# Kernel optimization log

Hardware: AMD Instinct MI355X
Metric: run time of the kernel (lower is better)

## Reference

```python
import jax, jax.numpy as jnp
import numpy as np

B, C, H, W = 4, 192, 56, 56
D_STATE, D_CONV, EXPAND = 16, 3, 2
D_INNER = EXPAND * C
DT_RANK = (C + 15) // 16  # 12


def setup_inputs() -> dict:
    key = jax.random.key(0)
    ks = jax.random.split(key, 16)
    s = 0.02
    return {
        "x": jax.random.normal(ks[0], (B, C, H, W), jnp.float32),
        "ln1_g": jnp.ones((C,), jnp.float32),
        "ln1_b": jnp.zeros((C,), jnp.float32),
        "in_proj_w": jax.random.normal(ks[1], (2 * D_INNER, C), jnp.float32) * s,
        "conv1d_w": jax.random.normal(ks[2], (D_INNER, 1, D_CONV), jnp.float32) * s,
        "conv1d_b": jnp.zeros((D_INNER,), jnp.float32),
        "x_proj_w": jax.random.normal(ks[3], (DT_RANK + 2 * D_STATE, D_INNER), jnp.float32) * s,
        "dt_proj_w": jax.random.normal(ks[4], (D_INNER, DT_RANK), jnp.float32) * (DT_RANK ** -0.5),
        "dt_proj_b": jax.random.uniform(ks[5], (D_INNER,), jnp.float32, -4.6, -2.3),
        "A_log": jnp.tile(jnp.log(jnp.arange(1, D_STATE + 1, dtype=jnp.float32)), (D_INNER, 1)),
        "Dskip": jnp.ones((D_INNER,), jnp.float32),
        "out_proj_w": jax.random.normal(ks[6], (C, D_INNER), jnp.float32) * s,
        "dw_w": jax.random.normal(ks[7], (C, 1, 3, 3), jnp.float32) * s,
        "bn_g": jnp.ones((C,), jnp.float32),
        "bn_b": jnp.zeros((C,), jnp.float32),
        "bn_mean": jax.random.normal(ks[8], (C,), jnp.float32) * 0.1,
        "bn_var": jax.random.uniform(ks[9], (C,), jnp.float32, 0.5, 1.5),
        "ln2_g": jnp.ones((C,), jnp.float32),
        "ln2_b": jnp.zeros((C,), jnp.float32),
        "mlp_w1": jax.random.normal(ks[10], (4 * C, C), jnp.float32) * s,
        "mlp_b1": jnp.zeros((4 * C,), jnp.float32),
        "mlp_w2": jax.random.normal(ks[11], (C, 4 * C), jnp.float32) * s,
        "mlp_b2": jnp.zeros((C,), jnp.float32),
    }


def _ln(x, g, b, eps=1e-5):
    m = jnp.mean(x, -1, keepdims=True)
    v = jnp.var(x, -1, keepdims=True)
    return (x - m) * jax.lax.rsqrt(v + eps) * g + b


def _gelu(x):
    return jax.nn.gelu(x, approximate=False)


def _mamba(xf, in_proj_w, conv1d_w, conv1d_b, x_proj_w, dt_proj_w, dt_proj_b, A_log, Dskip, out_proj_w):
    # xf: (B, L, C) tokens
    Bn, L, _ = xf.shape
    xz = jnp.einsum('blc,ec->ble', xf, in_proj_w)  # (B, L, 2*d_inner)
    xm, z = jnp.split(xz, 2, axis=-1)
    # causal depthwise conv1d over L
    xm_t = jnp.transpose(xm, (0, 2, 1))  # (B, d_inner, L)
    conv = jax.lax.conv_general_dilated(
        xm_t, conv1d_w, (1,), [(D_CONV - 1, 0)],
        feature_group_count=D_INNER,
        dimension_numbers=('NCH', 'OIH', 'NCH'))
    xm = jax.nn.silu(jnp.transpose(conv + conv1d_b[None, :, None], (0, 2, 1)))  # (B, L, d_inner)
    x_dbl = jnp.einsum('bld,ed->ble', xm, x_proj_w)
    dt = x_dbl[..., :DT_RANK]
    Bm = x_dbl[..., DT_RANK:DT_RANK + D_STATE]   # (B, L, n)
    Cm = x_dbl[..., DT_RANK + D_STATE:]          # (B, L, n)
    delta = jax.nn.softplus(jnp.einsum('blr,dr->bld', dt, dt_proj_w) + dt_proj_b)
    A = -jnp.exp(A_log)                           # (d_inner, n)
    deltaA = jnp.exp(delta[..., None] * A)        # (B, L, d, n)
    deltaBx = (delta * xm)[..., None] * Bm[:, :, None, :]  # (B, L, d, n)

    def step(h, inp):
        dA, dBx, Ct = inp
        h = dA * h + dBx                          # (B, d, n)
        y = jnp.einsum('bdn,bn->bd', h, Ct)
        return h, y

    h0 = jnp.zeros((Bn, D_INNER, D_STATE), xm.dtype)
    _, ys = jax.lax.scan(step, h0, (jnp.transpose(deltaA, (1, 0, 2, 3)),
                                    jnp.transpose(deltaBx, (1, 0, 2, 3)),
                                    jnp.transpose(Cm, (1, 0, 2))))
    y = jnp.transpose(ys, (1, 0, 2)) + xm * Dskip  # (B, L, d_inner)
    y = y * jax.nn.silu(z)
    return jnp.einsum('bld,cd->blc', y, out_proj_w)


def reference(x, ln1_g, ln1_b, in_proj_w, conv1d_w, conv1d_b, x_proj_w, dt_proj_w, dt_proj_b,
              A_log, Dskip, out_proj_w, dw_w, bn_g, bn_b, bn_mean, bn_var,
              ln2_g, ln2_b, mlp_w1, mlp_b1, mlp_w2, mlp_b2):
    Bn, Cn, Hn, Wn = x.shape
    # --- branch 1: LN -> SS2D (Mamba over flattened tokens) + skip
    t = jnp.transpose(x, (0, 2, 3, 1))            # (B, H, W, C)
    t = _ln(t, ln1_g, ln1_b)
    tokens = t.reshape(Bn, Hn * Wn, Cn)           # row-major = rearrange 'b c h w -> b (h w) c' after LN
    y = _mamba(tokens, in_proj_w, conv1d_w, conv1d_b, x_proj_w, dt_proj_w, dt_proj_b,
               A_log, Dskip, out_proj_w)
    x1 = x + jnp.transpose(y.reshape(Bn, Hn, Wn, Cn), (0, 3, 1, 2))
    # --- branch 2: depthwise conv -> BN(eval) -> GELU + skip
    dw = jax.lax.conv_general_dilated(x1, dw_w, (1, 1), [(1, 1), (1, 1)],
                                      feature_group_count=Cn,
                                      dimension_numbers=('NCHW', 'OIHW', 'NCHW'))
    bn = (dw - bn_mean[None, :, None, None]) * jax.lax.rsqrt(bn_var + 1e-5)[None, :, None, None]
    bn = bn * bn_g[None, :, None, None] + bn_b[None, :, None, None]
    x2 = x1 + _gelu(bn)
    # --- branch 3: LN -> MLP + skip
    t = jnp.transpose(x2, (0, 2, 3, 1))
    t = _ln(t, ln2_g, ln2_b)
    h = _gelu(jnp.einsum('bhwc,ec->bhwe', t, mlp_w1) + mlp_b1)
    m = jnp.einsum('bhwe,ce->bhwc', h, mlp_w2) + mlp_b2
    return x2 + jnp.transpose(m, (0, 3, 1, 2))
```

## Files before the change

### kernel.cpp

```cpp
#include <hip/hip_runtime.h>
#include <hip/hip_bf16.h>
#include <math.h>

#define BATCH 4
#define CCH   192
#define HH    56
#define WW    56
#define LSEQ  (HH*WW)
#define NTOK  (BATCH*LSEQ)
#define DST   16
#define DIN   384
#define DTR   12
#define NXC   416
#define CL    32
#define NC    (LSEQ/CL)

typedef __attribute__((ext_vector_type(8))) short short8;
typedef __attribute__((ext_vector_type(4))) short short4v;
typedef __attribute__((ext_vector_type(4))) float floatx4;

__device__ __forceinline__ float siluf(float x)  { return x / (1.f + __expf(-x)); }
__device__ __forceinline__ float geluf(float x)  { return 0.5f * x * (1.f + erff(x * 0.70710678118654752f)); }
__device__ __forceinline__ float softplusf(float x) { return (x > 20.f) ? x : log1pf(__expf(x)); }
__device__ __forceinline__ float bf2f(short u) {
    union { unsigned int i; float f; } cv; cv.i = ((unsigned int)(unsigned short)u) << 16; return cv.f;
}
__device__ __forceinline__ short f2bf_bits(float v) {
    __hip_bfloat16 h = __float2bfloat16(v);
    return *(short*)&h;
}

#define WSZ0 147456
#define WSZ2 73728
#define WSZ3 147456
#define WSZ4 147456
__global__ __launch_bounds__(256) void cvt_weights(const float* __restrict__ w0,
                                                   const float* __restrict__ w2, const float* __restrict__ w3,
                                                   const float* __restrict__ w4,
                                                   __hip_bfloat16* __restrict__ o0,
                                                   __hip_bfloat16* __restrict__ o2, __hip_bfloat16* __restrict__ o3,
                                                   __hip_bfloat16* __restrict__ o4) {
    int i = blockIdx.x * 256 + threadIdx.x;
    if (i < WSZ0) { o0[i] = __float2bfloat16(w0[i]); return; } i -= WSZ0;
    if (i < WSZ2) { o2[i] = __float2bfloat16(w2[i]); return; } i -= WSZ2;
    if (i < WSZ3) { o3[i] = __float2bfloat16(w3[i]); return; } i -= WSZ3;
    if (i < WSZ4) { o4[i] = __float2bfloat16(w4[i]); }
}

__global__ __launch_bounds__(256) void make_wcomb(const float* __restrict__ xp_w,
                                                  const float* __restrict__ dt_w,
                                                  __hip_bfloat16* __restrict__ wcomb) {
    int i = blockIdx.x * 256 + threadIdx.x;
    if (i >= NXC * DIN) return;
    int row = i / DIN, k = i % DIN;
    float v;
    if (row < DIN) {
        v = 0.f;
#pragma unroll
        for (int r = 0; r < DTR; r++) v += dt_w[row * DTR + r] * xp_w[r * DIN + k];
    } else {
        v = xp_w[(row - DIN + DTR) * DIN + k];
    }
    wcomb[i] = __float2bfloat16(v);
}

__global__ __launch_bounds__(256) void ln_kernel(const float* __restrict__ x,
                                                 const float* __restrict__ g,
                                                 const float* __restrict__ bta,
                                                 __hip_bfloat16* __restrict__ out) {
    __shared__ float tile[CCH * 65];
    __shared__ float gs[CCH], bs[CCH];
    int t = threadIdx.x;
    int b = blockIdx.y, hw0 = blockIdx.x * 64;
    const float* xb = x + (size_t)b * CCH * LSEQ + hw0;
#pragma unroll 8
    for (int k = 0; k < 48; k++) {
        int idx = k * 256 + t;
        int c = idx >> 6, w = idx & 63;
        tile[c * 65 + w] = xb[(size_t)c * LSEQ + w];
    }
    if (t < CCH) { gs[t] = g[t]; bs[t] = bta[t]; }
    __syncthreads();
    int lane = t & 63, wave = t >> 6;
    int tk = lane & 15, p = lane >> 4;
    int tok = wave * 16 + tk;
    float s = 0.f, s2 = 0.f;
#pragma unroll 8
    for (int i = 0; i < 48; i++) {
        float v = tile[(p * 48 + i) * 65 + tok];
        s += v; s2 += v * v;
    }
    s += __shfl_xor(s, 16); s2 += __shfl_xor(s2, 16);
    s += __shfl_xor(s, 32); s2 += __shfl_xor(s2, 32);
    float mean = s * (1.f / CCH);
    float rstd = rsqrtf(s2 * (1.f / CCH) - mean * mean + 1e-5f);
    int j = lane >> 2, q = lane & 3;
    float mj = __shfl(mean, j);
    float rj = __shfl(rstd, j);
    int wtok = wave * 16 + j;
    __hip_bfloat16* op = out + (size_t)(b * LSEQ + hw0 + wtok) * CCH + q * 48;
#pragma unroll
    for (int kk = 0; kk < 6; kk++) {
        short8 pk;
#pragma unroll
        for (int e = 0; e < 8; e++) {
            int c = q * 48 + kk * 8 + e;
            float v = (tile[c * 65 + wtok] - mj) * rj * gs[c] + bs[c];
            pk[e] = f2bf_bits(v);
        }
        *(short8*)(op + kk * 8) = pk;
    }
}

template<int EPI, typename OutT>
__global__ __launch_bounds__(256) void gemm_mfma(const __hip_bfloat16* __restrict__ A,
                                                 const __hip_bfloat16* __restrict__ W,
                                                 const float* __restrict__ bias,
                                                 const float* __restrict__ res,
                                                 OutT* __restrict__ Cout,
                                                 float* __restrict__ aux,
                                                 int N, int K) {
    __shared__ __align__(16) __hip_bfloat16 AsBs[2][2][64 * 40];
    int tid = threadIdx.x;
    int bm = blockIdx.y * 64, bn = blockIdx.x * 64;
    int wave = tid >> 6, lane = tid & 63;
    int wm = (wave >> 1) * 32, wn = (wave & 1) * 32;
    int lm = lane & 15, quad = lane >> 4;
    floatx4 acc[2][2] = {};
    int lrow = tid >> 2;
    int lcol = (tid & 3) * 8;
    const int nk = K >> 5;
    short8 zero8 = {0,0,0,0,0,0,0,0};
    short8 ra, rb;
    ra = *(const short8*)(A + (size_t)(bm + lrow) * K + lcol);
    {
        int n0 = bn + lrow;
        rb = (n0 < N) ? *(const short8*)(W + (size_t)n0 * K + lcol) : zero8;
    }
    *(short8*)&AsBs[0][0][lrow * 40 + lcol] = ra;
    *(short8*)&AsBs[0][1][lrow * 40 + lcol] = rb;
    __syncthreads();
    for (int kk = 0; kk < nk; kk++) {
        int cur = kk & 1;
        bool more = (kk + 1 < nk);
        if (more) {
            int k0 = (kk + 1) * 32;
            ra = *(const short8*)(A + (size_t)(bm + lrow) * K + k0 + lcol);
            int n0 = bn + lrow;
            rb = (n0 < N) ? *(const short8*)(W + (size_t)n0 * K + k0 + lcol) : zero8;
        }
        short8 a[2], b[2];
#pragma unroll
        for (int i = 0; i < 2; i++) a[i] = *(const short8*)&AsBs[cur][0][(wm + i * 16 + lm) * 40 + quad * 8];
#pragma unroll
        for (int j = 0; j < 2; j++) b[j] = *(const short8*)&AsBs[cur][1][(wn + j * 16 + lm) * 40 + quad * 8];
#pragma unroll
        for (int i = 0; i < 2; i++)
#pragma unroll
            for (int j = 0; j < 2; j++)
                acc[i][j] = __builtin_amdgcn_mfma_f32_16x16x32_bf16(a[i], b[j], acc[i][j], 0, 0, 0);
        if (more) {
            int nxt = cur ^ 1;
            *(short8*)&AsBs[nxt][0][lrow * 40 + lcol] = ra;
            *(short8*)&AsBs[nxt][1][lrow * 40 + lcol] = rb;
        }
        __syncthreads();
    }
    if constexpr (EPI == 3 || EPI == 4) {
#pragma unroll
        for (int j = 0; j < 2; j++) {
            int n = bn + wn + j * 16 + lm;
            if (n >= N) continue;
            float bv = (EPI == 4) ? bias[n] : 0.f;
#pragma unroll
            for (int i = 0; i < 2; i++) {
                int mrow = bm + wm + i * 16 + quad * 4;
                int bb = mrow / LSEQ;
                int l0 = mrow % LSEQ;
                size_t oidx = ((size_t)(bb * CCH + n)) * LSEQ + l0;
                float4 xr = *(const float4*)(res + oidx);
                float4 v;
                v.x = acc[i][j][0] + bv + xr.x;
                v.y = acc[i][j][1] + bv + xr.y;
                v.z = acc[i][j][2] + bv + xr.z;
                v.w = acc[i][j][3] + bv + xr.w;
                *(float4*)((float*)Cout + oidx) = v;
            }
        }
        return;
    } else {
        __hip_bfloat16* tb = (__hip_bfloat16*)&AsBs[0][0][0];
        bool has_tile = (EPI != 5) || (bn < DIN);
        if (has_tile) {
#pragma unroll
            for (int j = 0; j < 2; j++) {
                int n = bn + wn + j * 16 + lm;
                float bv = (EPI == 2 || EPI == 5) ? bias[n] : 0.f;
#pragma unroll
                for (int i = 0; i < 2; i++) {
#pragma unroll
                    for (int r = 0; r < 4; r++) {
                        float v = acc[i][j][r];
                        if (EPI == 2) v = geluf(v + bv);
                        if (EPI == 5) v = softplusf(v + bv);
                        tb[(wm + i * 16 + quad * 4 + r) * 72 + wn + j * 16 + lm] = __float2bfloat16(v);
                    }
                }
            }
        }
        __syncthreads();
        if (has_tile) {
            int ldc = (EPI == 5) ? DIN : N;
            __hip_bfloat16* cb = (__hip_bfloat16*)Cout;
#pragma unroll
            for (int pass = 0; pass < 2; pass++) {
                int idx = pass * 256 + tid;
                int row = idx >> 3, chunk = idx & 7;
                short8 v = *(const short8*)&tb[row * 72 + chunk * 8];
                *(short8*)(cb + (size_t)(bm + row) * ldc + bn + chunk * 8) = v;
            }
        }
        if constexpr (EPI == 5) {
            if (bn >= DIN) {
#pragma unroll
                for (int j = 0; j < 2; j++) {
                    int n = bn + wn + j * 16 + lm;
                    if (n >= N) continue;
                    int nb = n - DIN;
#pragma unroll
                    for (int i = 0; i < 2; i++) {
                        int mrow = bm + wm + i * 16 + quad * 4;
#pragma unroll
                        for (int r = 0; r < 4; r++)
                            aux[(size_t)(mrow + r) * 32 + nb] = acc[i][j][r];
                    }
                }
            }
        }
    }
}

__global__ __launch_bounds__(256) void conv1d_silu(const __hip_bfloat16* __restrict__ xz,
                                                   const float* __restrict__ w,
                                                   const float* __restrict__ bias,
                                                   __hip_bfloat16* __restrict__ out_bf) {
    int idx = blockIdx.x * 256 + threadIdx.x;
    if (idx >= NTOK * (DIN / 4)) return;
    int m = idx / (DIN / 4), d = (idx % (DIN / 4)) * 4;
    int l = m % LSEQ;
    short4v cur = *(const short4v*)&xz[(size_t)m * (2 * DIN) + d];
    short4v p1 = {0,0,0,0}, p2 = {0,0,0,0};
    if (l >= 1) p1 = *(const short4v*)&xz[(size_t)(m - 1) * (2 * DIN) + d];
    if (l >= 2) p2 = *(const short4v*)&xz[(size_t)(m - 2) * (2 * DIN) + d];
    float4 bv = *(const float4*)&bias[d];
    short4v obv;
#pragma unroll
    for (int jj = 0; jj < 4; jj++) {
        float w0 = w[(d + jj) * 3 + 0], w1 = w[(d + jj) * 3 + 1], w2 = w[(d + jj) * 3 + 2];
        float acc = ((const float*)&bv)[jj] + w2 * bf2f(cur[jj]) + w1 * bf2f(p1[jj]) + w0 * bf2f(p2[jj]);
        obv[jj] = f2bf_bits(siluf(acc));
    }
    *(short4v*)&out_bf[(size_t)m * DIN + d] = obv;
}

__global__ __launch_bounds__(256) void scan_phase1(const __hip_bfloat16* __restrict__ delta,
                                                   const __hip_bfloat16* __restrict__ xm,
                                                   const float* __restrict__ bc,
                                                   const float* __restrict__ A_log,
                                                   float* __restrict__ Pbuf,
                                                   float* __restrict__ Qbuf) {
    __shared__ float b_s[CL][16];
    int t = threadIdx.x;
    int b = blockIdx.z, c = blockIdx.x, d0 = blockIdx.y * 128;
    int m0 = b * LSEQ + c * CL;
    {
        int i = t >> 3, q = (t & 7) * 2;
        *(float2*)&b_s[i][q] = *(const float2*)&bc[(size_t)(m0 + i) * 32 + q];
    }
    __syncthreads();
    int d = d0 + (t >> 1), half = t & 1;
    float An[8];
#pragma unroll
    for (int n4 = 0; n4 < 2; n4++) {
        float4 a = *(const float4*)&A_log[d * DST + half * 8 + n4 * 4];
        An[n4 * 4 + 0] = -__expf(a.x);
        An[n4 * 4 + 1] = -__expf(a.y);
        An[n4 * 4 + 2] = -__expf(a.z);
        An[n4 * 4 + 3] = -__expf(a.w);
    }
    float Q[8];
#pragma unroll
    for (int n = 0; n < 8; n++) Q[n] = 0.f;
    float s = 0.f;
    const __hip_bfloat16* dp = delta + (size_t)m0 * DIN + d;
    const __hip_bfloat16* xp = xm    + (size_t)m0 * DIN + d;
#pragma unroll 4
    for (int i = 0; i < CL; i++) {
        float dlt = bf2f(*(const short*)(dp + (size_t)i * DIN));
        float xv  = bf2f(*(const short*)(xp + (size_t)i * DIN));
        s += dlt;
        float tt = dlt * xv;
#pragma unroll
        for (int n = 0; n < 8; n++) {
            float dA = __expf(dlt * An[n]);
            Q[n] = dA * Q[n] + tt * b_s[i][half * 8 + n];
        }
    }
    size_t o = ((size_t)(b * NC + c) * DIN + d) * DST + half * 8;
#pragma unroll
    for (int n4 = 0; n4 < 2; n4++) {
        float4 Pv, Qv;
        Pv.x = __expf(An[n4 * 4 + 0] * s);
        Pv.y = __expf(An[n4 * 4 + 1] * s);
        Pv.z = __expf(An[n4 * 4 + 2] * s);
        Pv.w = __expf(An[n4 * 4 + 3] * s);
        Qv.x = Q[n4 * 4 + 0]; Qv.y = Q[n4 * 4 + 1];
        Qv.z = Q[n4 * 4 + 2]; Qv.w = Q[n4 * 4 + 3];
        *(float4*)&Pbuf[o + n4 * 4] = Pv;
        *(float4*)&Qbuf[o + n4 * 4] = Qv;
    }
}

__global__ __launch_bounds__(256) void scan_phase2(const float* __restrict__ Pbuf,
                                                   const float* __restrict__ Qbuf,
                                                   float* __restrict__ Hin) {
    int t = blockIdx.x * 256 + threadIdx.x;
    if (t >= BATCH * DIN * DST) return;
    int b = t / (DIN * DST);
    int rem = t % (DIN * DST);
    float h = 0.f;
#pragma unroll 7
    for (int c = 0; c < NC; c++) {
        size_t o = (size_t)(b * NC + c) * (DIN * DST) + rem;
        Hin[o] = h;
        h = Pbuf[o] * h + Qbuf[o];
    }
}

__global__ __launch_bounds__(256) void scan_phase3(const __hip_bfloat16* __restrict__ delta,
                                                   const __hip_bfloat16* __restrict__ xm,
                                                   const float* __restrict__ bc,
                                                   const __hip_bfloat16* __restrict__ xz,
                                                   const float* __restrict__ A_log,
                                                   const float* __restrict__ Dskip,
                                                   const float* __restrict__ Hin,
                                                   __hip_bfloat16* __restrict__ ybuf) {
    __shared__ float bc_s[CL][32];
    int t = threadIdx.x;
    int b = blockIdx.z, c = blockIdx.x, d0 = blockIdx.y * 128;
    int m0 = b * LSEQ + c * CL;
    {
        int i = t >> 3, q = (t & 7) * 4;
        *(float4*)&bc_s[i][q] = *(const float4*)&bc[(size_t)(m0 + i) * 32 + q];
    }
    __syncthreads();
    int d = d0 + (t >> 1), half = t & 1;
    float An[8];
#pragma unroll
    for (int n4 = 0; n4 < 2; n4++) {
        float4 a = *(const float4*)&A_log[d * DST + half * 8 + n4 * 4];
        An[n4 * 4 + 0] = -__expf(a.x);
        An[n4 * 4 + 1] = -__expf(a.y);
        An[n4 * 4 + 2] = -__expf(a.z);
        An[n4 * 4 + 3] = -__expf(a.w);
    }
    float h[8];
    size_t o = ((size_t)(b * NC + c) * DIN + d) * DST + half * 8;
    {
        float4 h0 = *(const float4*)&Hin[o];
        float4 h1 = *(const float4*)&Hin[o + 4];
        h[0] = h0.x; h[1] = h0.y; h[2] = h0.z; h[3] = h0.w;
        h[4] = h1.x; h[5] = h1.y; h[6] = h1.z; h[7] = h1.w;
    }
    float Dv = Dskip[d];
    const __hip_bfloat16* dp = delta + (size_t)m0 * DIN + d;
    const __hip_bfloat16* xp = xm    + (size_t)m0 * DIN + d;
    const __hip_bfloat16* zp = xz + (size_t)m0 * (2 * DIN) + DIN + d;
    __hip_bfloat16* yo = ybuf + (size_t)m0 * DIN + d;
#pragma unroll 2
    for (int i = 0; i < CL; i++) {
        float dlt = bf2f(*(const short*)(dp + (size_t)i * DIN));
        float xv  = bf2f(*(const short*)(xp + (size_t)i * DIN));
        float tt = dlt * xv;
        float y = 0.f;
#pragma unroll
        for (int n = 0; n < 8; n++) {
            float dA = __expf(dlt * An[n]);
            h[n] = dA * h[n] + tt * bc_s[i][half * 8 + n];
            y += h[n] * bc_s[i][16 + half * 8 + n];
        }
        y += __shfl_xor(y, 1);
        if (half == 0) {
            float zv = bf2f(*(const short*)(zp + (size_t)i * (2 * DIN)));
            yo[(size_t)i * DIN] = __float2bfloat16((y + xv * Dv) * siluf(zv));
        }
    }
}

__global__ __launch_bounds__(256) void dwconv_bn_gelu(const float* __restrict__ x1,
                                                      const float* __restrict__ wdw,
                                                      const float* __restrict__ bn_g,
                                                      const float* __restrict__ bn_b,
                                                      const float* __restrict__ bn_mean,
                                                      const float* __restrict__ bn_var,
                                                      float* __restrict__ x2) {
    int idx = blockIdx.x * 256 + threadIdx.x;
    if (idx >= NTOK * CCH / 4) return;
    int w4 = idx % (WW / 4); int tmp = idx / (WW / 4);
    int h = tmp % HH; tmp /= HH;
    int c = tmp % CCH; int b = tmp / CCH;
    int w0 = w4 * 4;
    const float* base = x1 + ((size_t)(b * CCH + c)) * LSEQ;
    float acc[4] = {0.f, 0.f, 0.f, 0.f};
    float4 mid0;
#pragma unroll
    for (int dh = -1; dh <= 1; dh++) {
        int hh = h + dh;
        if (hh < 0 || hh >= HH) { if (dh == 0) mid0 = *(const float4*)&base[h * WW + w0]; continue; }
        const float* row = base + hh * WW;
        float4 mid = *(const float4*)&row[w0];
        if (dh == 0) mid0 = mid;
        float lft = (w0 > 0) ? row[w0 - 1] : 0.f;
        float rgt = (w0 + 4 < WW) ? row[w0 + 4] : 0.f;
        float wA = wdw[c * 9 + (dh + 1) * 3 + 0];
        float wB = wdw[c * 9 + (dh + 1) * 3 + 1];
        float wC = wdw[c * 9 + (dh + 1) * 3 + 2];
        float in0 = lft, in1 = mid.x, in2 = mid.y, in3 = mid.z, in4 = mid.w, in5 = rgt;
        acc[0] += wA * in0 + wB * in1 + wC * in2;
        acc[1] += wA * in1 + wB * in2 + wC * in3;
        acc[2] += wA * in2 + wB * in3 + wC * in4;
        acc[3] += wA * in3 + wB * in4 + wC * in5;
    }
    float mu = bn_mean[c], rv = rsqrtf(bn_var[c] + 1e-5f) * bn_g[c], bb = bn_b[c];
    float4 o;
    o.x = mid0.x + geluf((acc[0] - mu) * rv + bb);
    o.y = mid0.y + geluf((acc[1] - mu) * rv + bb);
    o.z = mid0.z + geluf((acc[2] - mu) * rv + bb);
    o.w = mid0.w + geluf((acc[3] - mu) * rv + bb);
    *(float4*)&x2[((size_t)(b * CCH + c)) * LSEQ + h * WW + w0] = o;
}

extern "C" void kernel_launch(void* const* d_in, const int* in_sizes, int n_in,
                              void* d_out, int out_size, void* d_ws, size_t ws_size,
                              hipStream_t stream) {
    const float* x         = (const float*)d_in[0];
    const float* ln1_g     = (const float*)d_in[1];
    const float* ln1_b     = (const float*)d_in[2];
    const float* in_proj_w = (const float*)d_in[3];
    const float* conv_w    = (const float*)d_in[4];
    const float* conv_b    = (const float*)d_in[5];
    const float* x_proj_w  = (const float*)d_in[6];
    const float* dt_proj_w = (const float*)d_in[7];
    const float* dt_proj_b = (const float*)d_in[8];
    const float* A_log     = (const float*)d_in[9];
    const float* Dskip     = (const float*)d_in[10];
    const float* out_proj_w= (const float*)d_in[11];
    const float* dw_w      = (const float*)d_in[12];
    const float* bn_g      = (const float*)d_in[13];
    const float* bn_b      = (const float*)d_in[14];
    const float* bn_mean   = (const float*)d_in[15];
    const float* bn_var    = (const float*)d_in[16];
    const float* ln2_g     = (const float*)d_in[17];
    const float* ln2_b     = (const float*)d_in[18];
    const float* mlp_w1    = (const float*)d_in[19];
    const float* mlp_b1    = (const float*)d_in[20];
    const float* mlp_w2    = (const float*)d_in[21];
    const float* mlp_b2    = (const float*)d_in[22];
    float* out = (float*)d_out;

    char* wsb = (char*)d_ws;
    __hip_bfloat16* xz_bf     = (__hip_bfloat16*)wsb;                 wsb += (size_t)NTOK * 768 * 2;
    __hip_bfloat16* xm_bf     = (__hip_bfloat16*)wsb;                 wsb += (size_t)NTOK * DIN * 2;
    __hip_bfloat16* delta_bf  = (__hip_bfloat16*)wsb;                 wsb += (size_t)NTOK * DIN * 2;
    float*          bc        = (float*)wsb;                          wsb += (size_t)NTOK * 32 * 4;
    float*          Pbuf      = (float*)wsb;                          wsb += (size_t)NTOK * 192 * 4;
    float*          Qbuf      = (float*)wsb;                          wsb += (size_t)NTOK * 192 * 4;
    float*          Hin       = (float*)wsb;                          wsb += (size_t)NTOK * 192 * 4;
    float*          x1        = (float*)wsb;                          wsb += (size_t)NTOK * CCH * 4;
    float*          x2        = (float*)wsb;                          wsb += (size_t)NTOK * CCH * 4;
    __hip_bfloat16* tokens_bf = (__hip_bfloat16*)wsb;                 wsb += (size_t)NTOK * CCH * 2;
    __hip_bfloat16* ybuf_bf   = (__hip_bfloat16*)wsb;                 wsb += (size_t)NTOK * DIN * 2;
    __hip_bfloat16* hidden_bf = (__hip_bfloat16*)wsb;                 wsb += (size_t)NTOK * 768 * 2;
    __hip_bfloat16* in_w_bf   = (__hip_bfloat16*)wsb;                 wsb += WSZ0 * 2;
    __hip_bfloat16* op_w_bf   = (__hip_bfloat16*)wsb;                 wsb += WSZ2 * 2;
    __hip_bfloat16* w1_bf     = (__hip_bfloat16*)wsb;                 wsb += WSZ3 * 2;
    __hip_bfloat16* w2_bf     = (__hip_bfloat16*)wsb;                 wsb += WSZ4 * 2;
    __hip_bfloat16* wcomb_bf  = (__hip_bfloat16*)wsb;                 wsb += (size_t)NXC * DIN * 2;

    cvt_weights<<<(WSZ0 + WSZ2 + WSZ3 + WSZ4 + 255) / 256, 256, 0, stream>>>(
        in_proj_w, out_proj_w, mlp_w1, mlp_w2, in_w_bf, op_w_bf, w1_bf, w2_bf);
    make_wcomb<<<(NXC * DIN + 255) / 256, 256, 0, stream>>>(x_proj_w, dt_proj_w, wcomb_bf);
    ln_kernel<<<dim3(LSEQ / 64, BATCH), 256, 0, stream>>>(x, ln1_g, ln1_b, tokens_bf);
    gemm_mfma<0, __hip_bfloat16><<<dim3(768 / 64, NTOK / 64), 256, 0, stream>>>(tokens_bf, in_w_bf, nullptr, nullptr, xz_bf, nullptr, 768, CCH);
    conv1d_silu<<<(NTOK * (DIN / 4) + 255) / 256, 256, 0, stream>>>(xz_bf, conv_w, conv_b, xm_bf);
    gemm_mfma<5, __hip_bfloat16><<<dim3(7, NTOK / 64), 256, 0, stream>>>(xm_bf, wcomb_bf, dt_proj_b, nullptr, delta_bf, bc, NXC, DIN);
    scan_phase1<<<dim3(NC, DIN / 128, BATCH), 256, 0, stream>>>(delta_bf, xm_bf, bc, A_log, Pbuf, Qbuf);
    scan_phase2<<<(BATCH * DIN * DST + 255) / 256, 256, 0, stream>>>(Pbuf, Qbuf, Hin);
    scan_phase3<<<dim3(NC, DIN / 128, BATCH), 256, 0, stream>>>(delta_bf, xm_bf, bc, xz_bf, A_log, Dskip, Hin, ybuf_bf);
    gemm_mfma<3, float><<<dim3(3, NTOK / 64), 256, 0, stream>>>(ybuf_bf, op_w_bf, nullptr, x, x1, nullptr, CCH, DIN);
    dwconv_bn_gelu<<<(NTOK * CCH / 4 + 255) / 256, 256, 0, stream>>>(x1, dw_w, bn_g, bn_b, bn_mean, bn_var, x2);
    ln_kernel<<<dim3(LSEQ / 64, BATCH), 256, 0, stream>>>(x2, ln2_g, ln2_b, tokens_bf);
    gemm_mfma<2, __hip_bfloat16><<<dim3(768 / 64, NTOK / 64), 256, 0, stream>>>(tokens_bf, w1_bf, mlp_b1, nullptr, hidden_bf, nullptr, 768, CCH);
    gemm_mfma<4, float><<<dim3(3, NTOK / 64), 256, 0, stream>>>(hidden_bf, w2_bf, mlp_b2, x2, out, nullptr, CCH, 4 * CCH);
}
```

Before: 293.7 us.

## Fuse three scan phases into one persistent kernel with grid barriers

The three selective-scan phases (chunk summaries, cross-chunk carry, chunk output) now run in one kernel. Two atomic-counter grid barriers separate them, and the counters are cleared with a memset each call. The chunk length doubles to 64, which halves the carry buffers and the grid to 588 blocks. The two weight-prep kernels are also merged into one launch. This removes launch gaps and reloads of per-chunk state. The risk is a deadlock if not all blocks are resident at once, plus idle blocks during the serial carry phase and less parallelism in phases 1 and 3.

```diff
diff --git a/kernel.cpp b/kernel.cpp
--- a/kernel.cpp
+++ b/kernel.cpp
@@ -12,8 +12,9 @@
 #define DIN   384
 #define DTR   12
 #define NXC   416
-#define CL    32
+#define CL    64
 #define NC    (LSEQ/CL)
+#define NBLK  (NC*3*BATCH)
 
 typedef __attribute__((ext_vector_type(8))) short short8;
 typedef __attribute__((ext_vector_type(4))) short short4v;
@@ -34,34 +35,32 @@
 #define WSZ2 73728
 #define WSZ3 147456
 #define WSZ4 147456
-__global__ __launch_bounds__(256) void cvt_weights(const float* __restrict__ w0,
-                                                   const float* __restrict__ w2, const float* __restrict__ w3,
-                                                   const float* __restrict__ w4,
-                                                   __hip_bfloat16* __restrict__ o0,
-                                                   __hip_bfloat16* __restrict__ o2, __hip_bfloat16* __restrict__ o3,
-                                                   __hip_bfloat16* __restrict__ o4) {
+#define WSZC (NXC*DIN)
+__global__ __launch_bounds__(256) void prep_weights(const float* __restrict__ w0,
+                                                    const float* __restrict__ w2, const float* __restrict__ w3,
+                                                    const float* __restrict__ w4,
+                                                    const float* __restrict__ xp_w, const float* __restrict__ dt_w,
+                                                    __hip_bfloat16* __restrict__ o0,
+                                                    __hip_bfloat16* __restrict__ o2, __hip_bfloat16* __restrict__ o3,
+                                                    __hip_bfloat16* __restrict__ o4,
+                                                    __hip_bfloat16* __restrict__ wcomb) {
     int i = blockIdx.x * 256 + threadIdx.x;
     if (i < WSZ0) { o0[i] = __float2bfloat16(w0[i]); return; } i -= WSZ0;
     if (i < WSZ2) { o2[i] = __float2bfloat16(w2[i]); return; } i -= WSZ2;
     if (i < WSZ3) { o3[i] = __float2bfloat16(w3[i]); return; } i -= WSZ3;
-    if (i < WSZ4) { o4[i] = __float2bfloat16(w4[i]); }
-}
-
-__global__ __launch_bounds__(256) void make_wcomb(const float* __restrict__ xp_w,
-                                                  const float* __restrict__ dt_w,
-                                                  __hip_bfloat16* __restrict__ wcomb) {
-    int i = blockIdx.x * 256 + threadIdx.x;
-    if (i >= NXC * DIN) return;
-    int row = i / DIN, k = i % DIN;
-    float v;
-    if (row < DIN) {
-        v = 0.f;
-#pragma unroll
-        for (int r = 0; r < DTR; r++) v += dt_w[row * DTR + r] * xp_w[r * DIN + k];
-    } else {
-        v = xp_w[(row - DIN + DTR) * DIN + k];
-    }
-    wcomb[i] = __float2bfloat16(v);
+    if (i < WSZ4) { o4[i] = __float2bfloat16(w4[i]); return; } i -= WSZ4;
+    if (i < WSZC) {
+        int row = i / DIN, k = i % DIN;
+        float v;
+        if (row < DIN) {
+            v = 0.f;
+#pragma unroll
+            for (int r = 0; r < DTR; r++) v += dt_w[row * DTR + r] * xp_w[r * DIN + k];
+        } else {
+            v = xp_w[(row - DIN + DTR) * DIN + k];
+        }
+        wcomb[i] = __float2bfloat16(v);
+    }
 }
 
 __global__ __launch_bounds__(256) void ln_kernel(const float* __restrict__ x,
@@ -263,19 +262,37 @@
     *(short4v*)&out_bf[(size_t)m * DIN + d] = obv;
 }
 
-__global__ __launch_bounds__(256) void scan_phase1(const __hip_bfloat16* __restrict__ delta,
-                                                   const __hip_bfloat16* __restrict__ xm,
-                                                   const float* __restrict__ bc,
-                                                   const float* __restrict__ A_log,
-                                                   float* __restrict__ Pbuf,
-                                                   float* __restrict__ Qbuf) {
-    __shared__ float b_s[CL][16];
+__device__ __forceinline__ void global_barrier(unsigned* cnt, unsigned target) {
+    __syncthreads();
+    if (threadIdx.x == 0) {
+        __threadfence();
+        atomicAdd(cnt, 1u);
+        while (__hip_atomic_load(cnt, __ATOMIC_ACQUIRE, __HIP_MEMORY_SCOPE_AGENT) < target) {
+            __builtin_amdgcn_s_sleep(8);
+        }
+    }
+    __syncthreads();
+}
+
+__global__ __launch_bounds__(256, 4) void scan_fused(const __hip_bfloat16* __restrict__ delta,
+                                                     const __hip_bfloat16* __restrict__ xm,
+                                                     const float* __restrict__ bc,
+                                                     const __hip_bfloat16* __restrict__ xz,
+                                                     const float* __restrict__ A_log,
+                                                     const float* __restrict__ Dskip,
+                                                     float* __restrict__ Pbuf,
+                                                     float* __restrict__ Qbuf,
+                                                     float* __restrict__ Hin,
+                                                     __hip_bfloat16* __restrict__ ybuf,
+                                                     unsigned* __restrict__ bar) {
+    __shared__ float bc_s[CL][32];
     int t = threadIdx.x;
     int b = blockIdx.z, c = blockIdx.x, d0 = blockIdx.y * 128;
     int m0 = b * LSEQ + c * CL;
     {
-        int i = t >> 3, q = (t & 7) * 2;
-        *(float2*)&b_s[i][q] = *(const float2*)&bc[(size_t)(m0 + i) * 32 + q];
+        int i = t >> 2, q = (t & 3) * 8;
+        *(float4*)&bc_s[i][q]     = *(const float4*)&bc[(size_t)(m0 + i) * 32 + q];
+        *(float4*)&bc_s[i][q + 4] = *(const float4*)&bc[(size_t)(m0 + i) * 32 + q + 4];
     }
     __syncthreads();
     int d = d0 + (t >> 1), half = t & 1;
@@ -303,7 +320,7 @@
 #pragma unroll
         for (int n = 0; n < 8; n++) {
             float dA = __expf(dlt * An[n]);
-            Q[n] = dA * Q[n] + tt * b_s[i][half * 8 + n];
+            Q[n] = dA * Q[n] + tt * bc_s[i][half * 8 + n];
         }
     }
     size_t o = ((size_t)(b * NC + c) * DIN + d) * DST + half * 8;
@@ -319,53 +336,24 @@
         *(float4*)&Pbuf[o + n4 * 4] = Pv;
         *(float4*)&Qbuf[o + n4 * 4] = Qv;
     }
-}
-
-__global__ __launch_bounds__(256) void scan_phase2(const float* __restrict__ Pbuf,
-                                                   const float* __restrict__ Qbuf,
-                                                   float* __restrict__ Hin) {
-    int t = blockIdx.x * 256 + threadIdx.x;
-    if (t >= BATCH * DIN * DST) return;
-    int b = t / (DIN * DST);
-    int rem = t % (DIN * DST);
-    float h = 0.f;
+    global_barrier(&bar[0], NBLK);
+    {
+        int fb = (blockIdx.z * gridDim.y + blockIdx.y) * gridDim.x + blockIdx.x;
+        int gt = fb * 256 + t;
+        if (gt < BATCH * DIN * DST) {
+            int bb = gt / (DIN * DST);
+            int rem = gt % (DIN * DST);
+            float h = 0.f;
 #pragma unroll 7
-    for (int c = 0; c < NC; c++) {
-        size_t o = (size_t)(b * NC + c) * (DIN * DST) + rem;
-        Hin[o] = h;
-        h = Pbuf[o] * h + Qbuf[o];
-    }
-}
-
-__global__ __launch_bounds__(256) void scan_phase3(const __hip_bfloat16* __restrict__ delta,
-                                                   const __hip_bfloat16* __restrict__ xm,
-                                                   const float* __restrict__ bc,
-                                                   const __hip_bfloat16* __restrict__ xz,
-                                                   const float* __restrict__ A_log,
-                                                   const float* __restrict__ Dskip,
-                                                   const float* __restrict__ Hin,
-                                                   __hip_bfloat16* __restrict__ ybuf) {
-    __shared__ float bc_s[CL][32];
-    int t = threadIdx.x;
-    int b = blockIdx.z, c = blockIdx.x, d0 = blockIdx.y * 128;
-    int m0 = b * LSEQ + c * CL;
-    {
-        int i = t >> 3, q = (t & 7) * 4;
-        *(float4*)&bc_s[i][q] = *(const float4*)&bc[(size_t)(m0 + i) * 32 + q];
-    }
-    __syncthreads();
-    int d = d0 + (t >> 1), half = t & 1;
-    float An[8];
-#pragma unroll
-    for (int n4 = 0; n4 < 2; n4++) {
-        float4 a = *(const float4*)&A_log[d * DST + half * 8 + n4 * 4];
-        An[n4 * 4 + 0] = -__expf(a.x);
-        An[n4 * 4 + 1] = -__expf(a.y);
-        An[n4 * 4 + 2] = -__expf(a.z);
-        An[n4 * 4 + 3] = -__expf(a.w);
-    }
+            for (int cc = 0; cc < NC; cc++) {
+                size_t oo = (size_t)(bb * NC + cc) * (DIN * DST) + rem;
+                Hin[oo] = h;
+                h = Pbuf[oo] * h + Qbuf[oo];
+            }
+        }
+    }
+    global_barrier(&bar[1], NBLK);
     float h[8];
-    size_t o = ((size_t)(b * NC + c) * DIN + d) * DST + half * 8;
     {
         float4 h0 = *(const float4*)&Hin[o];
         float4 h1 = *(const float4*)&Hin[o + 4];
@@ -373,8 +361,6 @@
         h[4] = h1.x; h[5] = h1.y; h[6] = h1.z; h[7] = h1.w;
     }
     float Dv = Dskip[d];
-    const __hip_bfloat16* dp = delta + (size_t)m0 * DIN + d;
-    const __hip_bfloat16* xp = xm    + (size_t)m0 * DIN + d;
     const __hip_bfloat16* zp = xz + (size_t)m0 * (2 * DIN) + DIN + d;
     __hip_bfloat16* yo = ybuf + (size_t)m0 * DIN + d;
 #pragma unroll 2
@@ -473,9 +459,9 @@
     __hip_bfloat16* xm_bf     = (__hip_bfloat16*)wsb;                 wsb += (size_t)NTOK * DIN * 2;
     __hip_bfloat16* delta_bf  = (__hip_bfloat16*)wsb;                 wsb += (size_t)NTOK * DIN * 2;
     float*          bc        = (float*)wsb;                          wsb += (size_t)NTOK * 32 * 4;
-    float*          Pbuf      = (float*)wsb;                          wsb += (size_t)NTOK * 192 * 4;
-    float*          Qbuf      = (float*)wsb;                          wsb += (size_t)NTOK * 192 * 4;
-    float*          Hin       = (float*)wsb;                          wsb += (size_t)NTOK * 192 * 4;
+    float*          Pbuf      = (float*)wsb;                          wsb += (size_t)NTOK * 96 * 4;
+    float*          Qbuf      = (float*)wsb;                          wsb += (size_t)NTOK * 96 * 4;
+    float*          Hin       = (float*)wsb;                          wsb += (size_t)NTOK * 96 * 4;
     float*          x1        = (float*)wsb;                          wsb += (size_t)NTOK * CCH * 4;
     float*          x2        = (float*)wsb;                          wsb += (size_t)NTOK * CCH * 4;
     __hip_bfloat16* tokens_bf = (__hip_bfloat16*)wsb;                 wsb += (size_t)NTOK * CCH * 2;
@@ -485,18 +471,18 @@
     __hip_bfloat16* op_w_bf   = (__hip_bfloat16*)wsb;                 wsb += WSZ2 * 2;
     __hip_bfloat16* w1_bf     = (__hip_bfloat16*)wsb;                 wsb += WSZ3 * 2;
     __hip_bfloat16* w2_bf     = (__hip_bfloat16*)wsb;                 wsb += WSZ4 * 2;
-    __hip_bfloat16* wcomb_bf  = (__hip_bfloat16*)wsb;                 wsb += (size_t)NXC * DIN * 2;
-
-    cvt_weights<<<(WSZ0 + WSZ2 + WSZ3 + WSZ4 + 255) / 256, 256, 0, stream>>>(
-        in_proj_w, out_proj_w, mlp_w1, mlp_w2, in_w_bf, op_w_bf, w1_bf, w2_bf);
-    make_wcomb<<<(NXC * DIN + 255) / 256, 256, 0, stream>>>(x_proj_w, dt_proj_w, wcomb_bf);
+    __hip_bfloat16* wcomb_bf  = (__hip_bfloat16*)wsb;                 wsb += (size_t)WSZC * 2;
+    unsigned*       bar       = (unsigned*)wsb;                       wsb += 2 * sizeof(unsigned);
+
+    hipMemsetAsync(bar, 0, 2 * sizeof(unsigned), stream);
+    prep_weights<<<(WSZ0 + WSZ2 + WSZ3 + WSZ4 + WSZC + 255) / 256, 256, 0, stream>>>(
+        in_proj_w, out_proj_w, mlp_w1, mlp_w2, x_proj_w, dt_proj_w,
+        in_w_bf, op_w_bf, w1_bf, w2_bf, wcomb_bf);
     ln_kernel<<<dim3(LSEQ / 64, BATCH), 256, 0, stream>>>(x, ln1_g, ln1_b, tokens_bf);
     gemm_mfma<0, __hip_bfloat16><<<dim3(768 / 64, NTOK / 64), 256, 0, stream>>>(tokens_bf, in_w_bf, nullptr, nullptr, xz_bf, nullptr, 768, CCH);
     conv1d_silu<<<(NTOK * (DIN / 4) + 255) / 256, 256, 0, stream>>>(xz_bf, conv_w, conv_b, xm_bf);
     gemm_mfma<5, __hip_bfloat16><<<dim3(7, NTOK / 64), 256, 0, stream>>>(xm_bf, wcomb_bf, dt_proj_b, nullptr, delta_bf, bc, NXC, DIN);
-    scan_phase1<<<dim3(NC, DIN / 128, BATCH), 256, 0, stream>>>(delta_bf, xm_bf, bc, A_log, Pbuf, Qbuf);
-    scan_phase2<<<(BATCH * DIN * DST + 255) / 256, 256, 0, stream>>>(Pbuf, Qbuf, Hin);
-    scan_phase3<<<dim3(NC, DIN / 128, BATCH), 256, 0, stream>>>(delta_bf, xm_bf, bc, xz_bf, A_log, Dskip, Hin, ybuf_bf);
+    scan_fused<<<dim3(NC, DIN / 128, BATCH), 256, 0, stream>>>(delta_bf, xm_bf, bc, xz_bf, A_log, Dskip, Pbuf, Qbuf, Hin, ybuf_bf, bar);
     gemm_mfma<3, float><<<dim3(3, NTOK / 64), 256, 0, stream>>>(ybuf_bf, op_w_bf, nullptr, x, x1, nullptr, CCH, DIN);
     dwconv_bn_gelu<<<(NTOK * CCH / 4 + 255) / 256, 256, 0, stream>>>(x1, dw_w, bn_g, bn_b, bn_mean, bn_var, x2);
     ln_kernel<<<dim3(LSEQ / 64, BATCH), 256, 0, stream>>>(x2, ln2_g, ln2_b, tokens_bf);
```

Measured after the change: 597.1 us. +103.3%, slower.
